# Optimization experiments

Measured on AMD Instinct MI355X. Metric: run time of the kernel, lower is better.

Reference implementation:

```python
import jax, jax.numpy as jnp
import numpy as np

EPS = 1e-6

def setup_inputs() -> dict:
    key = jax.random.key(0)
    ks = jax.random.split(key, 5)
    B, NH, S, DH = 2, 4, 2048, 128
    return {
        "q": jax.random.normal(ks[0], (B, NH, S, DH), dtype=jnp.float32),
        "k": jax.random.normal(ks[1], (B, NH, S, DH), dtype=jnp.float32),
        "v": jax.random.normal(ks[2], (B, NH, S, DH), dtype=jnp.float32),
        "i": jax.random.normal(ks[3], (B, NH, S), dtype=jnp.float32),
        "f": jax.random.normal(ks[4], (B, NH, S), dtype=jnp.float32),
    }

def _mlstm(q, k, v, i, f):
    # q,k,v: [B,NH,S,DH]; i,f: [B,NH,S] gate pre-activations.
    B, NH, S, DH = q.shape
    q = q * (DH ** -0.5)
    f_log = jax.nn.log_sigmoid(f)  # log forget gate

    # time-major for scan: [S, B, NH, ...]
    qT = jnp.moveaxis(q, 2, 0)
    kT = jnp.moveaxis(k, 2, 0)
    vT = jnp.moveaxis(v, 2, 0)
    iT = jnp.moveaxis(i, 2, 0)
    fT = jnp.moveaxis(f_log, 2, 0)

    C0 = jnp.zeros((B, NH, DH, DH), dtype=q.dtype)  # matrix memory C
    n0 = jnp.zeros((B, NH, DH), dtype=q.dtype)      # normalizer state n
    m0 = jnp.zeros((B, NH), dtype=q.dtype)          # max-stabilizer state m

    def step(carry, xs):
        C, n, m = carry
        q_t, k_t, v_t, i_t, fl_t = xs
        m_new = jnp.maximum(fl_t + m, i_t)               # [B,NH]
        a = jnp.exp(fl_t + m - m_new)                    # decay scale
        b = jnp.exp(i_t - m_new)                         # input scale
        C_new = a[..., None, None] * C + b[..., None, None] * (
            k_t[..., :, None] * v_t[..., None, :])       # [B,NH,DH,DH]
        n_new = a[..., None] * n + b[..., None] * k_t    # [B,NH,DH]
        h_num = jnp.einsum('bhd,bhde->bhe', q_t, C_new)  # [B,NH,DH]
        qn = jnp.einsum('bhd,bhd->bh', q_t, n_new)
        denom = jnp.maximum(jnp.abs(qn), jnp.exp(-m_new)) + EPS
        h = h_num / denom[..., None]
        return (C_new, n_new, m_new), h

    _, hT = jax.lax.scan(step, (C0, n0, m0), (qT, kT, vT, iT, fT))
    return jnp.moveaxis(hT, 0, 2)  # [B,NH,S,DH]

def reference(q, k, v, i, f):
    return _mlstm(q, k, v, i, f)
```

## Files before the change

kernel.cpp:

```cpp
#include <hip/hip_runtime.h>
#include <math.h>


typedef _Float16 f16;
typedef _Float16 f16x4 __attribute__((ext_vector_type(4)));
typedef _Float16 f16x8 __attribute__((ext_vector_type(8)));
typedef float    f32x4 __attribute__((ext_vector_type(4)));

#define S_LEN  2048
#define DHD    128
#define NHEADS 8
#define EPS    1e-6f

#define BUFSZ   65536
#define QNL_OFF 131072
#define SMEM_BYTES 131584

__device__ __forceinline__ int kswz(int row, int byteInRow) {
  return row * 256 + (byteInRow ^ ((row & 15) << 4));
}
__device__ __forceinline__ f32x4 mfma16(f16x8 a, f16x8 b, f32x4 c) {
  return __builtin_amdgcn_mfma_f32_16x16x32_f16(a, b, c, 0, 0, 0);
}
__device__ __forceinline__ void gload16(const void* g, void* l) {
  __builtin_amdgcn_global_load_lds((const __attribute__((address_space(1))) unsigned int*)g,
                                   (__attribute__((address_space(3))) unsigned int*)l, 16, 0, 0);
}

__global__ __launch_bounds__(256) void mlstm_scan(
    const float* __restrict__ ig_all, const float* __restrict__ fg_all,
    float* __restrict__ bf, float* __restrict__ Mf, float* __restrict__ en)
{
  const int hd  = blockIdx.x;
  const int tid = threadIdx.x;
  __shared__ double sc[256];
  const float* fg = fg_all + (size_t)hd * S_LEN;
  const float* ig = ig_all + (size_t)hd * S_LEN;
  const int base = tid * 8;

  double v[8];
#pragma unroll
  for (int u = 0; u < 8; ++u) {
    float x = fg[base + u];
    float fl = fminf(x, 0.0f) - log1pf(expf(-fabsf(x)));
    v[u] = (double)fl;
  }
#pragma unroll
  for (int u = 1; u < 8; ++u) v[u] += v[u - 1];
  sc[tid] = v[7];
  __syncthreads();
  for (int off = 1; off < 256; off <<= 1) {
    double t = (tid >= off) ? sc[tid - off] : 0.0;
    __syncthreads();
    sc[tid] += t;
    __syncthreads();
  }
  const double excl = sc[tid] - v[7];

  double F[8], b[8];
#pragma unroll
  for (int u = 0; u < 8; ++u) {
    F[u] = v[u] + excl;
    b[u] = (double)ig[base + u] - F[u];
    bf[(size_t)hd * S_LEN + base + u] = (float)b[u];
  }
  __syncthreads();
  double mv[8];
  mv[0] = b[0];
#pragma unroll
  for (int u = 1; u < 8; ++u) mv[u] = fmax(mv[u - 1], b[u]);
  sc[tid] = mv[7];
  __syncthreads();
  for (int off = 1; off < 256; off <<= 1) {
    double t = (tid >= off) ? sc[tid - off] : -1.0e300;
    __syncthreads();
    sc[tid] = fmax(sc[tid], t);
    __syncthreads();
  }
  const double exclm = (tid > 0) ? sc[tid - 1] : -1.0e300;
  double run = exclm;
#pragma unroll
  for (int u = 0; u < 8; ++u) {
    run = fmax(run, b[u]);
    double Mt = fmax(0.0, run);
    Mf[(size_t)hd * S_LEN + base + u] = (float)Mt;
    en[(size_t)hd * S_LEN + base + u] = (float)exp(-(F[u] + Mt));
  }
}

__global__ __launch_bounds__(256) void mlstm_prep(
    const float* __restrict__ kg, const float* __restrict__ vg,
    char* __restrict__ gkh, char* __restrict__ gkl,
    char* __restrict__ gvh, char* __restrict__ gvl)
{
  __shared__ float vts[64][132];
  const int bid = blockIdx.x;
  const int tid = threadIdx.x;

  if (bid < 256) {
    const int gid  = bid * 256 + tid;
    const int row  = gid >> 2;
    const int part = gid & 3;
    const float* src = kg + (size_t)row * DHD;
    char* oh = gkh + (size_t)row * 256;
    char* ol = gkl + (size_t)row * 256;
#pragma unroll
    for (int j = 0; j < 8; ++j) {
      float4 x = *(const float4*)(src + j * 16 + part * 4);
      float xs[4] = {x.x, x.y, x.z, x.w};
      f16x4 hi, lo;
#pragma unroll
      for (int s = 0; s < 4; ++s) { f16 h = (f16)xs[s]; hi[s] = h; lo[s] = (f16)(xs[s] - (float)h); }
      const int byte = (j * 32 + part * 8) ^ ((row & 15) << 4);
      *(f16x4*)(oh + byte) = hi;
      *(f16x4*)(ol + byte) = lo;
    }
  } else {
    const int b2   = bid - 256;
    const int head = b2 >> 5;
    const int it   = b2 & 31;
    {
      const int r   = tid >> 2;
      const int seg = tid & 3;
      const float* src = vg + ((size_t)(head * S_LEN + it * 64 + r)) * DHD;
#pragma unroll
      for (int j = 0; j < 8; ++j) {
        const int c4 = j * 16 + seg * 4;
        *(float4*)&vts[r][c4] = *(const float4*)(src + c4);
      }
    }
    __syncthreads();
    const int e = tid >> 1;
    const int h = tid & 1;
    const size_t tb = (size_t)(head * 32 + it) * 16384 + (size_t)e * 128;
#pragma unroll
    for (int i4 = 0; i4 < 8; ++i4) {
      f16x4 hi, lo;
#pragma unroll
      for (int s = 0; s < 4; ++s) {
        float x = vts[32 * h + i4 * 4 + s][e];
        f16 hh = (f16)x; hi[s] = hh; lo[s] = (f16)(x - (float)hh);
      }
      const int byte = ((32 * h + i4 * 4) * 2) ^ ((e & 15) << 3);
      *(f16x4*)(gvh + tb + byte) = hi;
      *(f16x4*)(gvl + tb + byte) = lo;
    }
  }
}

__global__ __launch_bounds__(256, 1) void mlstm_fast2(
    const float* __restrict__ qg,
    const char* __restrict__ gkh, const char* __restrict__ gkl,
    const char* __restrict__ gvh, const char* __restrict__ gvl,
    const float* __restrict__ bf, const float* __restrict__ Mf,
    const float* __restrict__ en, float* __restrict__ outg)
{
  extern __shared__ char smem[];
  const int bid  = blockIdx.x;
  const int hd   = bid & 7;
  const int j    = bid >> 3;
  const int t0   = j * 64;
  const int tid  = threadIdx.x;
  const int w    = tid >> 6;
  const int lane = tid & 63;
  const int c    = lane & 15;
  const int g    = lane >> 4;
  const int wk   = w & 1;
  const int qp   = w >> 1;

  const size_t hbase = (size_t)hd * S_LEN;
  const char* pkh = gkh + hbase * 256;
  const char* pkl = gkl + hbase * 256;
  const char* pvh = gvh + (size_t)hd * 524288;
  const char* pvl = gvl + (size_t)hd * 524288;

  const int n_it = j + 1;

  {
    const size_t tb = 0;
#pragma unroll
    for (int u = 0; u < 4; ++u) {
      const int off = (w << 12) + (u << 10);
      const int gl  = off + lane * 16;
      gload16(pkh + tb + gl, smem + 0     + off);
      gload16(pkl + tb + gl, smem + 16384 + off);
      gload16(pvh + tb + gl, smem + 32768 + off);
      gload16(pvl + tb + gl, smem + 49152 + off);
    }
  }

  constexpr float QSC = 0.08838834764831845f;
  f16x8 qfh[2][4], qfl[2][4];
#pragma unroll
  for (int u = 0; u < 2; ++u) {
    const float* qrow = qg + (hbase + t0 + 16 * (2 * qp + u) + c) * DHD;
#pragma unroll
    for (int kc = 0; kc < 4; ++kc) {
      const float* p = qrow + kc * 32 + 8 * g;
      float4 a = *(const float4*)p;
      float4 b = *(const float4*)(p + 4);
      float xs[8] = {a.x, a.y, a.z, a.w, b.x, b.y, b.z, b.w};
#pragma unroll
      for (int s = 0; s < 8; ++s) {
        float x = xs[s] * QSC;
        f16 hi = (f16)x;
        qfh[u][kc][s] = hi;
        qfl[u][kc][s] = (f16)(x - (float)hi);
      }
    }
  }
  float Mq[2];
  Mq[0] = Mf[hbase + t0 + 16 * (2 * qp) + c];
  Mq[1] = Mf[hbase + t0 + 16 * (2 * qp + 1) + c];

  const f32x4 z4 = {0.f, 0.f, 0.f, 0.f};
  f32x4 hacc[2][8];
#pragma unroll
  for (int u = 0; u < 2; ++u)
#pragma unroll
    for (int et = 0; et < 8; ++et) hacc[u][et] = z4;
  float qn[2] = {0.f, 0.f};

  int cur = 0;
  for (int it = 0; it < n_it; ++it) {
    const int s0 = it * 64;
    __syncthreads();

    f32x4 b0 = *(const f32x4*)(bf + hbase + s0 + 32 * wk + 4 * g);
    f32x4 b1 = *(const f32x4*)(bf + hbase + s0 + 32 * wk + 16 + 4 * g);

    if (it + 1 < n_it) {
      const size_t tb = (size_t)(it + 1) * 16384;
      char* lb = smem + (cur ^ 1) * BUFSZ;
#pragma unroll
      for (int u = 0; u < 4; ++u) {
        const int off = (w << 12) + (u << 10);
        const int gl  = off + lane * 16;
        gload16(pkh + tb + gl, lb + 0     + off);
        gload16(pkl + tb + gl, lb + 16384 + off);
        gload16(pvh + tb + gl, lb + 32768 + off);
        gload16(pvl + tb + gl, lb + 49152 + off);
      }
    }

    const char* lb = smem + cur * BUFSZ;

    f32x4 sacc[2][2];
    sacc[0][0] = z4; sacc[0][1] = z4; sacc[1][0] = z4; sacc[1][1] = z4;
#pragma unroll
    for (int kc = 0; kc < 4; ++kc) {
      const int cb = kc * 64 + 16 * g;
      f16x8 kh0 = *(const f16x8*)(lb + 0     + kswz(32 * wk + c,      cb));
      f16x8 kl0 = *(const f16x8*)(lb + 16384 + kswz(32 * wk + c,      cb));
      f16x8 kh1 = *(const f16x8*)(lb + 0     + kswz(32 * wk + 16 + c, cb));
      f16x8 kl1 = *(const f16x8*)(lb + 16384 + kswz(32 * wk + 16 + c, cb));
#pragma unroll
      for (int u = 0; u < 2; ++u) {
        sacc[u][0] = mfma16(kh0, qfh[u][kc], sacc[u][0]);
        sacc[u][0] = mfma16(kh0, qfl[u][kc], sacc[u][0]);
        sacc[u][0] = mfma16(kl0, qfh[u][kc], sacc[u][0]);
        sacc[u][1] = mfma16(kh1, qfh[u][kc], sacc[u][1]);
        sacc[u][1] = mfma16(kh1, qfl[u][kc], sacc[u][1]);
        sacc[u][1] = mfma16(kl1, qfh[u][kc], sacc[u][1]);
      }
    }

    f16x8 pfh[2], pfl[2];
#pragma unroll
    for (int u = 0; u < 2; ++u) {
      const int qglob = t0 + 16 * (2 * qp + u) + c;
#pragma unroll
      for (int r = 0; r < 4; ++r) {
        const int kv0 = s0 + 32 * wk + 4 * g + r;
        const int kv1 = kv0 + 16;
        float p0 = (kv0 <= qglob) ? __expf(b0[r] - Mq[u]) * sacc[u][0][r] : 0.f;
        float p1 = (kv1 <= qglob) ? __expf(b1[r] - Mq[u]) * sacc[u][1][r] : 0.f;
        qn[u] += p0 + p1;
        f16 h0 = (f16)p0; pfh[u][r]     = h0; pfl[u][r]     = (f16)(p0 - (float)h0);
        f16 h1 = (f16)p1; pfh[u][r + 4] = h1; pfl[u][r + 4] = (f16)(p1 - (float)h1);
      }
    }

    const int byte0 = (64 * wk + 8 * g)      ^ (c << 3);
    const int byte1 = (64 * wk + 32 + 8 * g) ^ (c << 3);
#pragma unroll
    for (int et = 0; et < 8; ++et) {
      const int eb = (16 * et + c) * 128;
      f16x4 vh0 = *(const f16x4*)(lb + 32768 + eb + byte0);
      f16x4 vh1 = *(const f16x4*)(lb + 32768 + eb + byte1);
      f16x4 vl0 = *(const f16x4*)(lb + 49152 + eb + byte0);
      f16x4 vl1 = *(const f16x4*)(lb + 49152 + eb + byte1);
      f16x8 vfh, vfl;
#pragma unroll
      for (int s = 0; s < 4; ++s) {
        vfh[s] = vh0[s]; vfh[s + 4] = vh1[s];
        vfl[s] = vl0[s]; vfl[s + 4] = vl1[s];
      }
#pragma unroll
      for (int u = 0; u < 2; ++u) {
        hacc[u][et] = mfma16(pfh[u], vfh, hacc[u][et]);
        hacc[u][et] = mfma16(pfh[u], vfl, hacc[u][et]);
        hacc[u][et] = mfma16(pfl[u], vfh, hacc[u][et]);
      }
    }
    cur ^= 1;
  }

#pragma unroll
  for (int u = 0; u < 2; ++u) {
    qn[u] += __shfl_xor(qn[u], 16);
    qn[u] += __shfl_xor(qn[u], 32);
  }
  __syncthreads();
  float* qnl  = (float*)(smem + QNL_OFF);
  float* part = (float*)smem;
  if (lane < 16) {
    qnl[(wk * 4 + 2 * qp + 0) * 16 + lane] = qn[0];
    qnl[(wk * 4 + 2 * qp + 1) * 16 + lane] = qn[1];
  }
#pragma unroll
  for (int u = 0; u < 2; ++u)
#pragma unroll
    for (int et = 0; et < 8; ++et)
#pragma unroll
      for (int r = 0; r < 4; ++r)
        part[(wk * 64 + 16 * (2 * qp + u) + 4 * g + r) * 132 + 16 * et + c] = hacc[u][et][r];
  __syncthreads();

  const int e4 = (tid & 31) * 4;
#pragma unroll
  for (int pass = 0; pass < 8; ++pass) {
    const int q = pass * 8 + (tid >> 5);
    const float* pa = part + q * 132 + e4;
    const float* pb = part + (64 + q) * 132 + e4;
    f32x4 s;
#pragma unroll
    for (int s_ = 0; s_ < 4; ++s_) s[s_] = pa[s_] + pb[s_];
    const float qns = qnl[(q >> 4) * 16 + (q & 15)] + qnl[(4 + (q >> 4)) * 16 + (q & 15)];
    const float den = fmaxf(fabsf(qns), en[hbase + t0 + q]) + EPS;
    const float inv = 1.0f / den;
    float4 o = make_float4(s[0] * inv, s[1] * inv, s[2] * inv, s[3] * inv);
    *(float4*)(outg + (hbase + t0 + q) * DHD + e4) = o;
  }
}

extern "C" void kernel_launch(void* const* d_in, const int* in_sizes, int n_in,
                              void* d_out, int out_size, void* d_ws, size_t ws_size,
                              hipStream_t stream) {
  (void)in_sizes; (void)n_in; (void)out_size; (void)ws_size;
  const float* q  = (const float*)d_in[0];
  const float* k  = (const float*)d_in[1];
  const float* v  = (const float*)d_in[2];
  const float* ii = (const float*)d_in[3];
  const float* ff = (const float*)d_in[4];
  float* out = (float*)d_out;

  float* bf = (float*)d_ws;
  float* Mf = bf + NHEADS * S_LEN;
  float* en = Mf + NHEADS * S_LEN;

  const size_t PANEL = 4u * 1024 * 1024;
  char* gkh = (char*)(en + NHEADS * S_LEN);
  char* gkl = gkh + PANEL;
  char* gvh = gkl + PANEL;
  char* gvl = gvh + PANEL;

  hipFuncSetAttribute(reinterpret_cast<const void*>(mlstm_fast2),
                      hipFuncAttributeMaxDynamicSharedMemorySize, SMEM_BYTES);
  mlstm_scan<<<dim3(NHEADS), dim3(256), 0, stream>>>(ii, ff, bf, Mf, en);
  mlstm_prep<<<dim3(512), dim3(256), 0, stream>>>(k, v, gkh, gkl, gvh, gvl);
  mlstm_fast2<<<dim3(256), dim3(256), SMEM_BYTES, stream>>>(
      q, gkh, gkl, gvh, gvl, bf, Mf, en, out);
}
```

Measured before the change: 164.0 us.

## Split long causal tiles across two blocks, merge partials, fuse prep kernels

Query tiles 16-31, which have the most causal KV iterations, are now split across two blocks covering KV halves. Their partial numerators and normalizers go to the workspace and a new merge kernel combines and normalizes them. The main kernel drops the double-buffered 128KB LDS for a single 64KB buffer with launch_bounds(256,2) so two blocks can share a CU, and the scan and prep kernels are fused into one launch. In exchange, loads are no longer overlapped with compute, and the split adds an extra kernel and workspace traffic.

After: 136.3 us. 16.9% less time.

```diff
diff --git a/kernel.cpp b/kernel.cpp
--- a/kernel.cpp
+++ b/kernel.cpp
@@ -12,9 +12,12 @@
 #define NHEADS 8
 #define EPS    1e-6f
 
-#define BUFSZ   65536
-#define QNL_OFF 131072
-#define SMEM_BYTES 131584
+#define KHI 0
+#define KLO 16384
+#define VHI 32768
+#define VLO 49152
+#define QNL_OFF 65536
+#define SMEM_MAIN 66048
 
 __device__ __forceinline__ int kswz(int row, int byteInRow) {
   return row * 256 + (byteInRow ^ ((row & 15) << 4));
@@ -27,73 +30,15 @@
                                    (__attribute__((address_space(3))) unsigned int*)l, 16, 0, 0);
 }
 
-__global__ __launch_bounds__(256) void mlstm_scan(
+__global__ __launch_bounds__(256) void mlstm_pre(
+    const float* __restrict__ kg, const float* __restrict__ vg,
     const float* __restrict__ ig_all, const float* __restrict__ fg_all,
+    char* __restrict__ gkh, char* __restrict__ gkl,
+    char* __restrict__ gvh, char* __restrict__ gvl,
     float* __restrict__ bf, float* __restrict__ Mf, float* __restrict__ en)
 {
-  const int hd  = blockIdx.x;
-  const int tid = threadIdx.x;
+  __shared__ float vts[64][132];
   __shared__ double sc[256];
-  const float* fg = fg_all + (size_t)hd * S_LEN;
-  const float* ig = ig_all + (size_t)hd * S_LEN;
-  const int base = tid * 8;
-
-  double v[8];
-#pragma unroll
-  for (int u = 0; u < 8; ++u) {
-    float x = fg[base + u];
-    float fl = fminf(x, 0.0f) - log1pf(expf(-fabsf(x)));
-    v[u] = (double)fl;
-  }
-#pragma unroll
-  for (int u = 1; u < 8; ++u) v[u] += v[u - 1];
-  sc[tid] = v[7];
-  __syncthreads();
-  for (int off = 1; off < 256; off <<= 1) {
-    double t = (tid >= off) ? sc[tid - off] : 0.0;
-    __syncthreads();
-    sc[tid] += t;
-    __syncthreads();
-  }
-  const double excl = sc[tid] - v[7];
-
-  double F[8], b[8];
-#pragma unroll
-  for (int u = 0; u < 8; ++u) {
-    F[u] = v[u] + excl;
-    b[u] = (double)ig[base + u] - F[u];
-    bf[(size_t)hd * S_LEN + base + u] = (float)b[u];
-  }
-  __syncthreads();
-  double mv[8];
-  mv[0] = b[0];
-#pragma unroll
-  for (int u = 1; u < 8; ++u) mv[u] = fmax(mv[u - 1], b[u]);
-  sc[tid] = mv[7];
-  __syncthreads();
-  for (int off = 1; off < 256; off <<= 1) {
-    double t = (tid >= off) ? sc[tid - off] : -1.0e300;
-    __syncthreads();
-    sc[tid] = fmax(sc[tid], t);
-    __syncthreads();
-  }
-  const double exclm = (tid > 0) ? sc[tid - 1] : -1.0e300;
-  double run = exclm;
-#pragma unroll
-  for (int u = 0; u < 8; ++u) {
-    run = fmax(run, b[u]);
-    double Mt = fmax(0.0, run);
-    Mf[(size_t)hd * S_LEN + base + u] = (float)Mt;
-    en[(size_t)hd * S_LEN + base + u] = (float)exp(-(F[u] + Mt));
-  }
-}
-
-__global__ __launch_bounds__(256) void mlstm_prep(
-    const float* __restrict__ kg, const float* __restrict__ vg,
-    char* __restrict__ gkh, char* __restrict__ gkl,
-    char* __restrict__ gvh, char* __restrict__ gvl)
-{
-  __shared__ float vts[64][132];
   const int bid = blockIdx.x;
   const int tid = threadIdx.x;
 
@@ -115,7 +60,7 @@
       *(f16x4*)(oh + byte) = hi;
       *(f16x4*)(ol + byte) = lo;
     }
-  } else {
+  } else if (bid < 512) {
     const int b2   = bid - 256;
     const int head = b2 >> 5;
     const int it   = b2 & 31;
@@ -145,21 +90,84 @@
       *(f16x4*)(gvh + tb + byte) = hi;
       *(f16x4*)(gvl + tb + byte) = lo;
     }
-  }
-}
-
-__global__ __launch_bounds__(256, 1) void mlstm_fast2(
+  } else {
+    const int hd = bid - 512;
+    const float* fg = fg_all + (size_t)hd * S_LEN;
+    const float* ig = ig_all + (size_t)hd * S_LEN;
+    const int base = tid * 8;
+    double v[8];
+#pragma unroll
+    for (int u = 0; u < 8; ++u) {
+      float x = fg[base + u];
+      float fl = fminf(x, 0.0f) - log1pf(expf(-fabsf(x)));
+      v[u] = (double)fl;
+    }
+#pragma unroll
+    for (int u = 1; u < 8; ++u) v[u] += v[u - 1];
+    sc[tid] = v[7];
+    __syncthreads();
+    for (int off = 1; off < 256; off <<= 1) {
+      double t = (tid >= off) ? sc[tid - off] : 0.0;
+      __syncthreads();
+      sc[tid] += t;
+      __syncthreads();
+    }
+    const double excl = sc[tid] - v[7];
+    double F[8], b[8];
+#pragma unroll
+    for (int u = 0; u < 8; ++u) {
+      F[u] = v[u] + excl;
+      b[u] = (double)ig[base + u] - F[u];
+      bf[(size_t)hd * S_LEN + base + u] = (float)b[u];
+    }
+    __syncthreads();
+    double mv[8];
+    mv[0] = b[0];
+#pragma unroll
+    for (int u = 1; u < 8; ++u) mv[u] = fmax(mv[u - 1], b[u]);
+    sc[tid] = mv[7];
+    __syncthreads();
+    for (int off = 1; off < 256; off <<= 1) {
+      double t = (tid >= off) ? sc[tid - off] : -1.0e300;
+      __syncthreads();
+      sc[tid] = fmax(sc[tid], t);
+      __syncthreads();
+    }
+    const double exclm = (tid > 0) ? sc[tid - 1] : -1.0e300;
+    double run = exclm;
+#pragma unroll
+    for (int u = 0; u < 8; ++u) {
+      run = fmax(run, b[u]);
+      double Mt = fmax(0.0, run);
+      Mf[(size_t)hd * S_LEN + base + u] = (float)Mt;
+      en[(size_t)hd * S_LEN + base + u] = (float)exp(-(F[u] + Mt));
+    }
+  }
+}
+
+__global__ __launch_bounds__(256, 2) void mlstm_main(
     const float* __restrict__ qg,
     const char* __restrict__ gkh, const char* __restrict__ gkl,
     const char* __restrict__ gvh, const char* __restrict__ gvl,
     const float* __restrict__ bf, const float* __restrict__ Mf,
-    const float* __restrict__ en, float* __restrict__ outg)
+    const float* __restrict__ en, float* __restrict__ outg,
+    float* __restrict__ qn0, float* __restrict__ qn1,
+    float* __restrict__ partials, int use_split)
 {
-  extern __shared__ char smem[];
+  __shared__ char smem[SMEM_MAIN];
   const int bid  = blockIdx.x;
   const int hd   = bid & 7;
-  const int j    = bid >> 3;
-  const int t0   = j * 64;
+  int tile, it0, nit, mode;
+  if (!use_split) {
+    tile = bid >> 3; it0 = 0; nit = tile + 1; mode = 0;
+  } else if (bid < 128) {
+    tile = bid >> 3; it0 = 0; nit = tile + 1; mode = 0;
+  } else if (bid < 256) {
+    tile = 31 - ((bid >> 3) - 16); it0 = 0; nit = 16; mode = 1;
+  } else {
+    const int j = (bid - 256) >> 3; tile = 31 - j; it0 = 16; nit = 16 - j; mode = 2;
+  }
+  const int t0   = tile * 64;
   const int tid  = threadIdx.x;
   const int w    = tid >> 6;
   const int lane = tid & 63;
@@ -174,21 +182,6 @@
   const char* pvh = gvh + (size_t)hd * 524288;
   const char* pvl = gvl + (size_t)hd * 524288;
 
-  const int n_it = j + 1;
-
-  {
-    const size_t tb = 0;
-#pragma unroll
-    for (int u = 0; u < 4; ++u) {
-      const int off = (w << 12) + (u << 10);
-      const int gl  = off + lane * 16;
-      gload16(pkh + tb + gl, smem + 0     + off);
-      gload16(pkl + tb + gl, smem + 16384 + off);
-      gload16(pvh + tb + gl, smem + 32768 + off);
-      gload16(pvl + tb + gl, smem + 49152 + off);
-    }
-  }
-
   constexpr float QSC = 0.08838834764831845f;
   f16x8 qfh[2][4], qfl[2][4];
 #pragma unroll
@@ -221,39 +214,35 @@
     for (int et = 0; et < 8; ++et) hacc[u][et] = z4;
   float qn[2] = {0.f, 0.f};
 
-  int cur = 0;
-  for (int it = 0; it < n_it; ++it) {
+  for (int it = it0; it < it0 + nit; ++it) {
     const int s0 = it * 64;
     __syncthreads();
 
-    f32x4 b0 = *(const f32x4*)(bf + hbase + s0 + 32 * wk + 4 * g);
-    f32x4 b1 = *(const f32x4*)(bf + hbase + s0 + 32 * wk + 16 + 4 * g);
-
-    if (it + 1 < n_it) {
-      const size_t tb = (size_t)(it + 1) * 16384;
-      char* lb = smem + (cur ^ 1) * BUFSZ;
+    {
+      const size_t tb = (size_t)it * 16384;
 #pragma unroll
       for (int u = 0; u < 4; ++u) {
         const int off = (w << 12) + (u << 10);
         const int gl  = off + lane * 16;
-        gload16(pkh + tb + gl, lb + 0     + off);
-        gload16(pkl + tb + gl, lb + 16384 + off);
-        gload16(pvh + tb + gl, lb + 32768 + off);
-        gload16(pvl + tb + gl, lb + 49152 + off);
-      }
-    }
-
-    const char* lb = smem + cur * BUFSZ;
+        gload16(pkh + tb + gl, smem + KHI + off);
+        gload16(pkl + tb + gl, smem + KLO + off);
+        gload16(pvh + tb + gl, smem + VHI + off);
+        gload16(pvl + tb + gl, smem + VLO + off);
+      }
+    }
+    f32x4 b0 = *(const f32x4*)(bf + hbase + s0 + 32 * wk + 4 * g);
+    f32x4 b1 = *(const f32x4*)(bf + hbase + s0 + 32 * wk + 16 + 4 * g);
+    __syncthreads();
 
     f32x4 sacc[2][2];
     sacc[0][0] = z4; sacc[0][1] = z4; sacc[1][0] = z4; sacc[1][1] = z4;
 #pragma unroll
     for (int kc = 0; kc < 4; ++kc) {
       const int cb = kc * 64 + 16 * g;
-      f16x8 kh0 = *(const f16x8*)(lb + 0     + kswz(32 * wk + c,      cb));
-      f16x8 kl0 = *(const f16x8*)(lb + 16384 + kswz(32 * wk + c,      cb));
-      f16x8 kh1 = *(const f16x8*)(lb + 0     + kswz(32 * wk + 16 + c, cb));
-      f16x8 kl1 = *(const f16x8*)(lb + 16384 + kswz(32 * wk + 16 + c, cb));
+      f16x8 kh0 = *(const f16x8*)(smem + KHI + kswz(32 * wk + c,      cb));
+      f16x8 kl0 = *(const f16x8*)(smem + KLO + kswz(32 * wk + c,      cb));
+      f16x8 kh1 = *(const f16x8*)(smem + KHI + kswz(32 * wk + 16 + c, cb));
+      f16x8 kl1 = *(const f16x8*)(smem + KLO + kswz(32 * wk + 16 + c, cb));
 #pragma unroll
       for (int u = 0; u < 2; ++u) {
         sacc[u][0] = mfma16(kh0, qfh[u][kc], sacc[u][0]);
@@ -286,10 +275,10 @@
 #pragma unroll
     for (int et = 0; et < 8; ++et) {
       const int eb = (16 * et + c) * 128;
-      f16x4 vh0 = *(const f16x4*)(lb + 32768 + eb + byte0);
-      f16x4 vh1 = *(const f16x4*)(lb + 32768 + eb + byte1);
-      f16x4 vl0 = *(const f16x4*)(lb + 49152 + eb + byte0);
-      f16x4 vl1 = *(const f16x4*)(lb + 49152 + eb + byte1);
+      f16x4 vh0 = *(const f16x4*)(smem + VHI + eb + byte0);
+      f16x4 vh1 = *(const f16x4*)(smem + VHI + eb + byte1);
+      f16x4 vl0 = *(const f16x4*)(smem + VLO + eb + byte0);
+      f16x4 vl1 = *(const f16x4*)(smem + VLO + eb + byte1);
       f16x8 vfh, vfl;
 #pragma unroll
       for (int s = 0; s < 4; ++s) {
@@ -303,7 +292,6 @@
         hacc[u][et] = mfma16(pfl[u], vfh, hacc[u][et]);
       }
     }
-    cur ^= 1;
   }
 
 #pragma unroll
@@ -311,43 +299,93 @@
     qn[u] += __shfl_xor(qn[u], 16);
     qn[u] += __shfl_xor(qn[u], 32);
   }
-  __syncthreads();
+  float* part = (float*)smem;
   float* qnl  = (float*)(smem + QNL_OFF);
-  float* part = (float*)smem;
-  if (lane < 16) {
-    qnl[(wk * 4 + 2 * qp + 0) * 16 + lane] = qn[0];
-    qnl[(wk * 4 + 2 * qp + 1) * 16 + lane] = qn[1];
-  }
-#pragma unroll
-  for (int u = 0; u < 2; ++u)
-#pragma unroll
-    for (int et = 0; et < 8; ++et)
-#pragma unroll
-      for (int r = 0; r < 4; ++r)
-        part[(wk * 64 + 16 * (2 * qp + u) + 4 * g + r) * 132 + 16 * et + c] = hacc[u][et][r];
-  __syncthreads();
-
-  const int e4 = (tid & 31) * 4;
-#pragma unroll
-  for (int pass = 0; pass < 8; ++pass) {
-    const int q = pass * 8 + (tid >> 5);
-    const float* pa = part + q * 132 + e4;
-    const float* pb = part + (64 + q) * 132 + e4;
-    f32x4 s;
-#pragma unroll
-    for (int s_ = 0; s_ < 4; ++s_) s[s_] = pa[s_] + pb[s_];
-    const float qns = qnl[(q >> 4) * 16 + (q & 15)] + qnl[(4 + (q >> 4)) * 16 + (q & 15)];
-    const float den = fmaxf(fabsf(qns), en[hbase + t0 + q]) + EPS;
-    const float inv = 1.0f / den;
-    float4 o = make_float4(s[0] * inv, s[1] * inv, s[2] * inv, s[3] * inv);
-    *(float4*)(outg + (hbase + t0 + q) * DHD + e4) = o;
+  const int pslot = hd * 16 + (tile - 16);
+
+#pragma unroll
+  for (int round = 0; round < 2; ++round) {
+    __syncthreads();
+    if (qp == round) {
+      if (lane < 16) {
+        qnl[(wk * 2 + 0) * 16 + lane] = qn[0];
+        qnl[(wk * 2 + 1) * 16 + lane] = qn[1];
+      }
+#pragma unroll
+      for (int u = 0; u < 2; ++u)
+#pragma unroll
+        for (int et = 0; et < 8; ++et)
+#pragma unroll
+          for (int r = 0; r < 4; ++r)
+            part[(wk * 32 + 16 * u + 4 * g + r) * 132 + 16 * et + c] = hacc[u][et][r];
+    }
+    __syncthreads();
+
+    const int q32  = tid >> 3;
+    const int cseg = (tid & 7) * 16;
+    const int rowg = t0 + round * 32 + q32;
+    const float qns = qnl[(q32 >> 4) * 16 + (q32 & 15)] +
+                      qnl[(2 + (q32 >> 4)) * 16 + (q32 & 15)];
+    const float* pa = part + q32 * 132 + cseg;
+    const float* pb = part + (32 + q32) * 132 + cseg;
+    float4 s[4];
+#pragma unroll
+    for (int k = 0; k < 4; ++k) {
+      float4 a = *(const float4*)(pa + 4 * k);
+      float4 b = *(const float4*)(pb + 4 * k);
+      s[k] = make_float4(a.x + b.x, a.y + b.y, a.z + b.z, a.w + b.w);
+    }
+    if (mode == 0) {
+      const float den = fmaxf(fabsf(qns), en[hbase + rowg]) + EPS;
+      const float inv = 1.0f / den;
+      float* dst = outg + (hbase + rowg) * DHD + cseg;
+#pragma unroll
+      for (int k = 0; k < 4; ++k)
+        *(float4*)(dst + 4 * k) = make_float4(s[k].x * inv, s[k].y * inv, s[k].z * inv, s[k].w * inv);
+    } else if (mode == 1) {
+      float* dst = outg + (hbase + rowg) * DHD + cseg;
+#pragma unroll
+      for (int k = 0; k < 4; ++k) *(float4*)(dst + 4 * k) = s[k];
+      if ((tid & 7) == 0) qn0[pslot * 64 + round * 32 + q32] = qns;
+    } else {
+      float* dst = partials + ((size_t)pslot * 64 + round * 32 + q32) * DHD + cseg;
+#pragma unroll
+      for (int k = 0; k < 4; ++k) *(float4*)(dst + 4 * k) = s[k];
+      if ((tid & 7) == 0) qn1[pslot * 64 + round * 32 + q32] = qns;
+    }
+  }
+}
+
+__global__ __launch_bounds__(256) void mlstm_merge(
+    float* __restrict__ outg, const float* __restrict__ partials,
+    const float* __restrict__ qn0, const float* __restrict__ qn1,
+    const float* __restrict__ en)
+{
+  const int pslot = blockIdx.x;
+  const int h     = pslot >> 4;
+  const int tile  = 16 + (pslot & 15);
+  const size_t rowbase = (size_t)h * S_LEN + tile * 64;
+  const int tid = threadIdx.x;
+  const int r   = tid >> 2;
+  const int c4  = (tid & 3) * 32;
+  const float qns = qn0[pslot * 64 + r] + qn1[pslot * 64 + r];
+  const float den = fmaxf(fabsf(qns), en[rowbase + r]) + EPS;
+  const float inv = 1.0f / den;
+  float* orow = outg + (rowbase + r) * DHD + c4;
+  const float* prow = partials + ((size_t)pslot * 64 + r) * DHD + c4;
+#pragma unroll
+  for (int k = 0; k < 8; ++k) {
+    float4 a = *(const float4*)(orow + 4 * k);
+    float4 b = *(const float4*)(prow + 4 * k);
+    *(float4*)(orow + 4 * k) =
+        make_float4((a.x + b.x) * inv, (a.y + b.y) * inv, (a.z + b.z) * inv, (a.w + b.w) * inv);
   }
 }
 
 extern "C" void kernel_launch(void* const* d_in, const int* in_sizes, int n_in,
                               void* d_out, int out_size, void* d_ws, size_t ws_size,
                               hipStream_t stream) {
-  (void)in_sizes; (void)n_in; (void)out_size; (void)ws_size;
+  (void)in_sizes; (void)n_in; (void)out_size;
   const float* q  = (const float*)d_in[0];
   const float* k  = (const float*)d_in[1];
   const float* v  = (const float*)d_in[2];
@@ -364,11 +402,18 @@
   char* gkl = gkh + PANEL;
   char* gvh = gkl + PANEL;
   char* gvl = gvh + PANEL;
-
-  hipFuncSetAttribute(reinterpret_cast<const void*>(mlstm_fast2),
-                      hipFuncAttributeMaxDynamicSharedMemorySize, SMEM_BYTES);
-  mlstm_scan<<<dim3(NHEADS), dim3(256), 0, stream>>>(ii, ff, bf, Mf, en);
-  mlstm_prep<<<dim3(512), dim3(256), 0, stream>>>(k, v, gkh, gkl, gvh, gvl);
-  mlstm_fast2<<<dim3(256), dim3(256), SMEM_BYTES, stream>>>(
-      q, gkh, gkl, gvh, gvl, bf, Mf, en, out);
-}
+  float* qn0 = (float*)(gvl + PANEL);
+  float* qn1 = qn0 + 128 * 64;
+  float* partials = qn1 + 128 * 64;
+
+  const size_t need = 3u * NHEADS * S_LEN * 4 + 4 * PANEL
+                    + 2u * 128 * 64 * 4 + (size_t)128 * 64 * DHD * 4;
+  const int use_split = (ws_size >= need) ? 1 : 0;
+
+  mlstm_pre<<<dim3(520), dim3(256), 0, stream>>>(k, v, ii, ff,
+                                                 gkh, gkl, gvh, gvl, bf, Mf, en);
+  mlstm_main<<<dim3(use_split ? 384 : 256), dim3(256), 0, stream>>>(
+      q, gkh, gkl, gvh, gvl, bf, Mf, en, out, qn0, qn1, partials, use_split);
+  if (use_split)
+    mlstm_merge<<<dim3(128), dim3(256), 0, stream>>>(out, partials, qn0, qn1, en);
+}
```
